# Performance work log

Hardware: AMD Instinct MI355X
Metric: run time of the kernel (lower is better)

Reference implementation:

```python
import jax, jax.numpy as jnp
import numpy as np


def setup_inputs() -> dict:
    key = jax.random.key(0)
    k_in, k_w = jax.random.split(key)
    input = jax.random.normal(k_in, (16, 64, 64, 512), dtype=jnp.float32)
    weight = jax.random.normal(k_w, (512, 512), dtype=jnp.float32)
    return {"input": input, "weight": weight}


def reference(input, weight):
    # Faithful to the torch source, including its quirky (weight*weight).sum(0)
    # (sum over the vocab axis -> (embed_dim,) vector, broadcast over vocab
    # columns; valid here because vocab_size == embed_dim).
    batch_dims, embed_dim = input.shape[:-1], input.shape[-1]
    x = input.reshape(-1, embed_dim)                     # (N, D)
    dists = -2.0 * jnp.einsum("nd,vd->nv", x, weight) + jnp.sum(weight * weight, axis=0)[None, :]
    idxes = jnp.argmin(dists, axis=1)                    # (N,)
    values = weight[idxes].reshape(*batch_dims, embed_dim)
    return values
```

## Files before the change

kernel.cpp:

```cpp
#include <hip/hip_runtime.h>


#define DIM   512
#define VOCAB 512
#define EPS_GAP 0.18f
#define RBATCH 8

typedef float f32x4 __attribute__((ext_vector_type(4)));
typedef _Float16 f16x8 __attribute__((ext_vector_type(8)));
typedef unsigned long long u64;

__device__ inline u64 packkey(float s, int v){
    unsigned u = __float_as_uint(s);
    u = (u & 0x80000000u) ? ~u : (u | 0x80000000u);
    return (((u64)u) << 32) | (unsigned)(~v);
}
__device__ inline float keyscore(u64 k){
    unsigned e = (unsigned)(k >> 32);
    return __uint_as_float((e & 0x80000000u) ? (e & 0x7fffffffu) : ~e);
}
__device__ inline int keyv(u64 k){ return (int)(~(unsigned)(k & 0xffffffffu)); }
__device__ inline u64 umax64(u64 a, u64 b){ return a > b ? a : b; }
__device__ inline u64 umin64(u64 a, u64 b){ return a < b ? a : b; }

__global__ void colsumsq_kernel(const float* __restrict__ w, float* __restrict__ c){
    const int v = blockIdx.x;
    const int lane = threadIdx.x;
    double s = 0.0;
    for (int i = lane; i < DIM; i += 64){
        const float wv = w[i * VOCAB + v];
        s += (double)wv * (double)wv;
    }
    #pragma unroll
    for (int m = 1; m <= 32; m <<= 1) s += __shfl_xor(s, m, 64);
    if (lane == 0) c[v] = (float)s;
}

__global__ void prep_w(const float* __restrict__ w,
                       _Float16* __restrict__ whc,
                       unsigned* __restrict__ cnt){
    const int i = blockIdx.x * 256 + threadIdx.x;
    const int v = i >> 9, k = i & 511;
    const int d = (k >> 5) * 16384 + ((k >> 3) & 3) * 4096 + v * 8 + (k & 7);
    whc[d] = (_Float16)w[i];
    if (i == 0) *cnt = 0u;
}

__launch_bounds__(256, 3)
__global__ void k1_scores(const float* __restrict__ x,
                          const _Float16* __restrict__ whc,
                          const float* __restrict__ cg,
                          const float* __restrict__ w,
                          float* __restrict__ out,
                          int* __restrict__ list,
                          unsigned* __restrict__ cnt){
    __shared__ u64 mergeK[32][4][2];
    __shared__ int idx_s[32];

    const int t = threadIdx.x;
    const int lane = t & 63, wv = t >> 6, quad = lane >> 4, lm = lane & 15;
    const int cb = wv << 7;
    const long rbase = (long)blockIdx.x * 32;
    const float* xblk = x + rbase * DIM;

    f32x4 acc[2][8];
    #pragma unroll
    for (int ct = 0; ct < 8; ++ct){
        const float bias = -0.5f * cg[cb + ct * 16 + lm];
        f32x4 z; z[0] = bias; z[1] = bias; z[2] = bias; z[3] = bias;
        acc[0][ct] = z; acc[1][ct] = z;
    }

    const float* ap0 = xblk + (long)(lm)      * DIM + quad * 8;
    const float* ap1 = xblk + (long)(16 + lm) * DIM + quad * 8;

    float4 ar0a = *(const float4*)(ap0);
    float4 ar0b = *(const float4*)(ap0 + 4);
    float4 ar1a = *(const float4*)(ap1);
    float4 ar1b = *(const float4*)(ap1 + 4);

    #pragma unroll 1
    for (int ch = 0; ch < 16; ++ch){
        f16x8 ah0, ah1;
        ah0[0]=(_Float16)ar0a.x; ah0[1]=(_Float16)ar0a.y; ah0[2]=(_Float16)ar0a.z; ah0[3]=(_Float16)ar0a.w;
        ah0[4]=(_Float16)ar0b.x; ah0[5]=(_Float16)ar0b.y; ah0[6]=(_Float16)ar0b.z; ah0[7]=(_Float16)ar0b.w;
        ah1[0]=(_Float16)ar1a.x; ah1[1]=(_Float16)ar1a.y; ah1[2]=(_Float16)ar1a.z; ah1[3]=(_Float16)ar1a.w;
        ah1[4]=(_Float16)ar1b.x; ah1[5]=(_Float16)ar1b.y; ah1[6]=(_Float16)ar1b.z; ah1[7]=(_Float16)ar1b.w;

        const int chn = (ch < 15) ? ch + 1 : 15;
        ar0a = *(const float4*)(ap0 + chn * 32);
        ar0b = *(const float4*)(ap0 + chn * 32 + 4);
        ar1a = *(const float4*)(ap1 + chn * 32);
        ar1b = *(const float4*)(ap1 + chn * 32 + 4);

        const _Float16* bb = whc + ch * 16384 + quad * 4096 + (cb + lm) * 8;
        #pragma unroll
        for (int ct = 0; ct < 8; ++ct){
            const f16x8 bh = *(const f16x8*)(bb + ct * 128);
            acc[0][ct] = __builtin_amdgcn_mfma_f32_16x16x32_f16(ah0, bh, acc[0][ct], 0, 0, 0);
            acc[1][ct] = __builtin_amdgcn_mfma_f32_16x16x32_f16(ah1, bh, acc[1][ct], 0, 0, 0);
        }
    }

    #pragma unroll
    for (int rt = 0; rt < 2; ++rt){
        #pragma unroll
        for (int reg = 0; reg < 4; ++reg){
            u64 b1 = 0, b2 = 0;
            #pragma unroll
            for (int ct = 0; ct < 8; ++ct){
                const u64 key = packkey(acc[rt][ct][reg], cb + ct * 16 + lm);
                if (key > b1){ b2 = b1; b1 = key; }
                else if (key > b2){ b2 = key; }
            }
            #pragma unroll
            for (int m = 1; m <= 8; m <<= 1){
                const u64 o1 = __shfl_xor(b1, m, 64);
                const u64 o2 = __shfl_xor(b2, m, 64);
                const u64 n1 = umax64(b1, o1);
                b2 = umax64(umin64(b1, o1), umax64(b2, o2));
                b1 = n1;
            }
            if (lm == 0){
                const int row = rt * 16 + quad * 4 + reg;
                mergeK[row][wv][0] = b1;
                mergeK[row][wv][1] = b2;
            }
        }
    }
    __syncthreads();
    if (t < 32){
        u64 p1 = mergeK[t][0][0], p2 = mergeK[t][0][1];
        #pragma unroll
        for (int i = 1; i < 4; ++i){
            const u64 q1 = mergeK[t][i][0], q2 = mergeK[t][i][1];
            const u64 n1 = umax64(p1, q1);
            p2 = umax64(umin64(p1, q1), umax64(p2, q2));
            p1 = n1;
        }
        idx_s[t] = keyv(p1);
        if (keyscore(p1) - keyscore(p2) < EPS_GAP){
            const unsigned p = atomicAdd(cnt, 1u);
            list[p] = (int)(rbase + t);
        }
    }
    __syncthreads();

    for (int rr = 0; rr < 32; rr += 2){
        const int row  = rr + (t >> 7);
        const int col  = (t & 127) << 2;
        const int vidx = idx_s[row];
        const float4 val = *(const float4*)(w + (long)vidx * DIM + col);
        *(float4*)(out + (rbase + row) * DIM + col) = val;
    }
}

__global__ void refine_rows(const float* __restrict__ x, const float* __restrict__ w,
                            const float* __restrict__ cg, const int* __restrict__ list,
                            const unsigned* __restrict__ cnt, float* __restrict__ out){
    __shared__ __align__(16) float xs[RBATCH][DIM];
    __shared__ u64 wk[RBATCH][4];
    __shared__ int bestv_s[RBATCH];
    const int t = threadIdx.x;
    const int lane = t & 63, wvq = t >> 6;
    const int n = (int)*cnt;
    for (int base = blockIdx.x * RBATCH; base < n; base += gridDim.x * RBATCH){
        const int m = (n - base < RBATCH) ? (n - base) : RBATCH;
        __syncthreads();
        for (int s = t; s < m * 128; s += 256){
            const int r = s >> 7, c = (s & 127) << 2;
            *(float4*)&xs[r][c] = *(const float4*)(x + (long)list[base + r] * DIM + c);
        }
        __syncthreads();
        u64 best[RBATCH];
        #pragma unroll
        for (int r = 0; r < RBATCH; ++r) best[r] = 0;
        #pragma unroll
        for (int vv = 0; vv < 2; ++vv){
            const int v = t + vv * 256;
            const float* wr = w + (long)v * DIM;
            float s[RBATCH];
            #pragma unroll
            for (int r = 0; r < RBATCH; ++r) s[r] = -0.5f * cg[v];
            for (int k = 0; k < DIM; k += 4){
                const float4 w4 = *(const float4*)(wr + k);
                #pragma unroll
                for (int r = 0; r < RBATCH; ++r){
                    const float4 x4 = *(const float4*)&xs[r][k];
                    s[r] = fmaf(w4.x, x4.x, s[r]);
                    s[r] = fmaf(w4.y, x4.y, s[r]);
                    s[r] = fmaf(w4.z, x4.z, s[r]);
                    s[r] = fmaf(w4.w, x4.w, s[r]);
                }
            }
            #pragma unroll
            for (int r = 0; r < RBATCH; ++r)
                best[r] = umax64(best[r], packkey(s[r], v));
        }
        #pragma unroll
        for (int r = 0; r < RBATCH; ++r){
            u64 b = best[r];
            #pragma unroll
            for (int mm = 1; mm <= 32; mm <<= 1) b = umax64(b, __shfl_xor(b, mm, 64));
            if (lane == 0) wk[r][wvq] = b;
        }
        __syncthreads();
        if (t < RBATCH){
            const u64 b = umax64(umax64(wk[t][0], wk[t][1]), umax64(wk[t][2], wk[t][3]));
            bestv_s[t] = keyv(b);
        }
        __syncthreads();
        for (int s = t; s < m * 128; s += 256){
            const int r = s >> 7, c = (s & 127) << 2;
            *(float4*)(out + (long)list[base + r] * DIM + c) =
                *(const float4*)(w + (long)bestv_s[r] * DIM + c);
        }
    }
}

__launch_bounds__(256)
__global__ void fallback_full(const float* __restrict__ x, const float* __restrict__ w,
                              float* __restrict__ out){
    __shared__ __align__(16) float As[16][68];
    __shared__ __align__(16) float Bs[16][VOCAB];
    __shared__ int   idx_sf[64];
    __shared__ float c_s[VOCAB];

    const int t  = threadIdx.x;
    const int tx = t & 31;
    const int ty = t >> 5;
    const long rbase = (long)blockIdx.x * 64;
    const float* xblk = x + rbase * DIM;

    for (int vv = t; vv < VOCAB; vv += 256){
        double s = 0.0;
        for (int i = 0; i < DIM; ++i){
            const float wvv = w[i * VOCAB + vv];
            s += (double)wvv * (double)wvv;
        }
        c_s[vv] = (float)s;
    }

    float acc[8][16];
    #pragma unroll
    for (int r = 0; r < 8; ++r)
        #pragma unroll
        for (int j = 0; j < 16; ++j) acc[r][j] = 0.0f;

    for (int k0 = 0; k0 < DIM; k0 += 16){
        __syncthreads();
        {
            const int r  = t >> 2;
            const int kq = (t & 3) << 2;
            const float4 a4 = *(const float4*)(xblk + (long)r * DIM + k0 + kq);
            As[kq + 0][r] = a4.x; As[kq + 1][r] = a4.y;
            As[kq + 2][r] = a4.z; As[kq + 3][r] = a4.w;
        }
        #pragma unroll
        for (int vb = 0; vb < 8; ++vb){
            const int v  = (t >> 2) + (vb << 6);
            const int kq = (t & 3) << 2;
            const float4 b4 = *(const float4*)(w + (long)v * DIM + k0 + kq);
            Bs[kq + 0][v] = b4.x; Bs[kq + 1][v] = b4.y;
            Bs[kq + 2][v] = b4.z; Bs[kq + 3][v] = b4.w;
        }
        __syncthreads();

        #pragma unroll
        for (int k = 0; k < 16; ++k){
            float a[8];
            const float4 a03 = *(const float4*)&As[k][ty * 8];
            const float4 a47 = *(const float4*)&As[k][ty * 8 + 4];
            a[0] = a03.x; a[1] = a03.y; a[2] = a03.z; a[3] = a03.w;
            a[4] = a47.x; a[5] = a47.y; a[6] = a47.z; a[7] = a47.w;
            float b[16];
            #pragma unroll
            for (int j = 0; j < 16; ++j) b[j] = Bs[k][tx + (j << 5)];
            #pragma unroll
            for (int r = 0; r < 8; ++r)
                #pragma unroll
                for (int j = 0; j < 16; ++j)
                    acc[r][j] = fmaf(a[r], b[j], acc[r][j]);
        }
    }

    #pragma unroll
    for (int r = 0; r < 8; ++r){
        float best = acc[r][0] - 0.5f * c_s[tx];
        int   bv   = tx;
        #pragma unroll
        for (int j = 1; j < 16; ++j){
            const float s = acc[r][j] - 0.5f * c_s[tx + (j << 5)];
            if (s > best){ best = s; bv = tx + (j << 5); }
        }
        unsigned u = __float_as_uint(best);
        u = (u & 0x80000000u) ? ~u : (u | 0x80000000u);
        u64 key = ((u64)u << 32) | (unsigned)(~(unsigned)bv);
        #pragma unroll
        for (int m = 1; m <= 16; m <<= 1){
            const u64 o = __shfl_xor(key, m, 64);
            if (o > key) key = o;
        }
        if (tx == 0) idx_sf[ty * 8 + r] = (int)(~(unsigned)(key & 0xFFFFFFFFull));
    }
    __syncthreads();

    for (int rr = 0; rr < 64; rr += 2){
        const int row  = rr + (t >> 7);
        const int col  = (t & 127) << 2;
        const int vidx = idx_sf[row];
        const float4 val = *(const float4*)(w + (long)vidx * DIM + col);
        *(float4*)(out + (rbase + row) * DIM + col) = val;
    }
}

extern "C" void kernel_launch(void* const* d_in, const int* in_sizes, int n_in,
                              void* d_out, int out_size, void* d_ws, size_t ws_size,
                              hipStream_t stream){
    const float* x = (const float*)d_in[0];
    const float* w = (const float*)d_in[1];
    float* out = (float*)d_out;
    const int rows = in_sizes[0] / DIM;

    const size_t whc_off  = 0;
    const size_t c_off    = whc_off + (size_t)DIM * VOCAB * 2;
    const size_t list_off = c_off   + (size_t)VOCAB * 4;
    const size_t cnt_off  = list_off + (size_t)rows * 4;
    const size_t need     = cnt_off + 16;

    if (ws_size >= need){
        _Float16* whc  = (_Float16*)((char*)d_ws + whc_off);
        float*    c    = (float*)((char*)d_ws + c_off);
        int*      list = (int*)((char*)d_ws + list_off);
        unsigned* cnt  = (unsigned*)((char*)d_ws + cnt_off);

        prep_w<<<(DIM * VOCAB) / 256, 256, 0, stream>>>(w, whc, cnt);
        colsumsq_kernel<<<VOCAB, 64, 0, stream>>>(w, c);
        k1_scores<<<rows / 32, 256, 0, stream>>>(x, whc, c, w, out, list, cnt);
        refine_rows<<<512, 256, 0, stream>>>(x, w, c, list, cnt, out);
    } else {
        fallback_full<<<rows / 64, 256, 0, stream>>>(x, w, out);
    }
}
```

Before: 354.8 us.

## Stage converted fp16 input tile in LDS and raise occupancy bound

The whole 32x512 input tile is loaded cooperatively with coalesced float4 reads, converted to fp16 once, and stored in shared memory in MFMA-friendly order. Previously each of the 4 waves loaded and converted the same rows itself from global memory. The main loop then reads A fragments from LDS. Launch bounds go from 3 to 4 blocks per SM, which tightens register limits and adds 32KB of LDS per block. The prefetch overlap of the old loop is lost.

```diff
diff --git a/kernel.cpp b/kernel.cpp
--- a/kernel.cpp
+++ b/kernel.cpp
@@ -46,7 +46,7 @@
     if (i == 0) *cnt = 0u;
 }
 
-__launch_bounds__(256, 3)
+__launch_bounds__(256, 4)
 __global__ void k1_scores(const float* __restrict__ x,
                           const _Float16* __restrict__ whc,
                           const float* __restrict__ cg,
@@ -54,6 +54,7 @@
                           float* __restrict__ out,
                           int* __restrict__ list,
                           unsigned* __restrict__ cnt){
+    __shared__ __align__(16) _Float16 Ah[16384];
     __shared__ u64 mergeK[32][4][2];
     __shared__ int idx_s[32];
 
@@ -71,32 +72,30 @@
         acc[0][ct] = z; acc[1][ct] = z;
     }
 
-    const float* ap0 = xblk + (long)(lm)      * DIM + quad * 8;
-    const float* ap1 = xblk + (long)(16 + lm) * DIM + quad * 8;
-
-    float4 ar0a = *(const float4*)(ap0);
-    float4 ar0b = *(const float4*)(ap0 + 4);
-    float4 ar1a = *(const float4*)(ap1);
-    float4 ar1b = *(const float4*)(ap1 + 4);
-
-    #pragma unroll 1
+    #pragma unroll 4
+    for (int jj = 0; jj < 16; ++jj){
+        const int j   = jj * 256 + t;
+        const int row = (j >> 3) & 31;
+        const int k4  = (j & 7) | ((j >> 8) << 3);
+        const int kk  = k4 << 2;
+        const float4 a4 = *(const float4*)(xblk + (long)row * DIM + kk);
+        union { _Float16 h[4]; ushort4 u; } cv;
+        cv.h[0] = (_Float16)a4.x;
+        cv.h[1] = (_Float16)a4.y;
+        cv.h[2] = (_Float16)a4.z;
+        cv.h[3] = (_Float16)a4.w;
+        const int d = (((kk >> 5) * 4 + ((kk >> 3) & 3)) * 32 + row) * 8 + (kk & 7);
+        *(ushort4*)&Ah[d] = cv.u;
+    }
+    __syncthreads();
+
     for (int ch = 0; ch < 16; ++ch){
-        f16x8 ah0, ah1;
-        ah0[0]=(_Float16)ar0a.x; ah0[1]=(_Float16)ar0a.y; ah0[2]=(_Float16)ar0a.z; ah0[3]=(_Float16)ar0a.w;
-        ah0[4]=(_Float16)ar0b.x; ah0[5]=(_Float16)ar0b.y; ah0[6]=(_Float16)ar0b.z; ah0[7]=(_Float16)ar0b.w;
-        ah1[0]=(_Float16)ar1a.x; ah1[1]=(_Float16)ar1a.y; ah1[2]=(_Float16)ar1a.z; ah1[3]=(_Float16)ar1a.w;
-        ah1[4]=(_Float16)ar1b.x; ah1[5]=(_Float16)ar1b.y; ah1[6]=(_Float16)ar1b.z; ah1[7]=(_Float16)ar1b.w;
-
-        const int chn = (ch < 15) ? ch + 1 : 15;
-        ar0a = *(const float4*)(ap0 + chn * 32);
-        ar0b = *(const float4*)(ap0 + chn * 32 + 4);
-        ar1a = *(const float4*)(ap1 + chn * 32);
-        ar1b = *(const float4*)(ap1 + chn * 32 + 4);
-
-        const _Float16* bb = whc + ch * 16384 + quad * 4096 + (cb + lm) * 8;
+        f16x8 ah0 = *(const f16x8*)&Ah[((ch * 4 + quad) * 32 + lm) * 8];
+        f16x8 ah1 = *(const f16x8*)&Ah[((ch * 4 + quad) * 32 + 16 + lm) * 8];
+        const _Float16* bb = whc + ch * 16384 + quad * 4096;
         #pragma unroll
         for (int ct = 0; ct < 8; ++ct){
-            const f16x8 bh = *(const f16x8*)(bb + ct * 128);
+            const f16x8 bh = *(const f16x8*)(bb + (cb + ct * 16 + lm) * 8);
             acc[0][ct] = __builtin_amdgcn_mfma_f32_16x16x32_f16(ah0, bh, acc[0][ct], 0, 0, 0);
             acc[1][ct] = __builtin_amdgcn_mfma_f32_16x16x32_f16(ah1, bh, acc[1][ct], 0, 0, 0);
         }
```

New measurement: 331.0 us. 6.7% less time.
